# Kernel tuning notes

Hardware: AMD Instinct MI355X
Metric: run time of the kernel (lower is better)

The kernel has to match this reference:

```python
import jax, jax.numpy as jnp
import numpy as np

B, S = 16, 4096
E_ENC, E_DEC, H = 1024, 1024, 512


def setup_inputs() -> dict:
    key = jax.random.key(0)
    ks = jax.random.split(key, 8)
    sc_e = 1.0 / np.sqrt(E_ENC)
    sc_d = 1.0 / np.sqrt(E_DEC)
    sc_h = 1.0 / np.sqrt(H)
    return {
        "encoder_hiddens": jax.random.normal(ks[0], (B, S, E_ENC), jnp.float32),
        "decoder_hidden": jax.random.normal(ks[1], (B, E_DEC), jnp.float32),
        "We": jax.random.uniform(ks[2], (E_ENC, H), jnp.float32, -sc_e, sc_e),
        "be": jax.random.uniform(ks[3], (H,), jnp.float32, -sc_e, sc_e),
        "Wd": jax.random.uniform(ks[4], (E_DEC, H), jnp.float32, -sc_d, sc_d),
        "bd": jax.random.uniform(ks[5], (H,), jnp.float32, -sc_d, sc_d),
        "Wo": jax.random.uniform(ks[6], (H, 1), jnp.float32, -sc_h, sc_h),
        "bo": jax.random.uniform(ks[7], (1,), jnp.float32, -sc_h, sc_h),
    }


def reference(encoder_hiddens, decoder_hidden, We, be, Wd, bd, Wo, bo):
    # Additive (Bahdanau) attention.
    # enc_proj: [B,S,H]; dec_proj: [B,1,H] broadcast over sequence.
    enc_proj = jnp.einsum("bse,eh->bsh", encoder_hiddens, We) + be
    dec_proj = jnp.einsum("bd,dh->bh", decoder_hidden, Wd) + bd
    e = jnp.tanh(enc_proj + dec_proj[:, None, :])          # [B,S,H]
    scores = jnp.einsum("bsh,h->bs", e, Wo[:, 0]) + bo[0]  # [B,S]
    attn = jax.nn.softmax(scores, axis=-1)                 # [B,S]
    context = jnp.einsum("bs,bse->be", attn, encoder_hiddens)  # [B,E_ENC]
    return context
```

## Files before the change

### kernel.cpp

```cpp
#include <hip/hip_runtime.h>
#include <hip/hip_bf16.h>
#include <math.h>

#define B_ 16
#define S_ 4096
#define E_ 1024
#define H_ 512

typedef short bf16x8 __attribute__((ext_vector_type(8)));
typedef unsigned short u16x8 __attribute__((ext_vector_type(8)));
typedef float f32x4 __attribute__((ext_vector_type(4)));

__device__ inline unsigned short f2bf(float x) {
    __hip_bfloat16 h = __float2bfloat16(x);
    return *(unsigned short*)&h;
}

__global__ __launch_bounds__(256) void we_transpose_kernel(
    const float* __restrict__ We, unsigned short* __restrict__ WeT) {
    __shared__ float sT[64][65];
    int k0 = (blockIdx.x >> 3) * 64;
    int n0 = (blockIdx.x & 7) * 64;
    int t = threadIdx.x;
#pragma unroll
    for (int p = 0; p < 16; ++p) {
        int idx = p * 256 + t;
        int k = idx >> 6, n = idx & 63;
        sT[n][k] = We[(size_t)(k0 + k) * H_ + n0 + n];
    }
    __syncthreads();
#pragma unroll
    for (int p = 0; p < 16; ++p) {
        int idx = p * 256 + t;
        int n = idx >> 6, k = idx & 63;
        WeT[(size_t)(n0 + n) * E_ + k0 + k] = f2bf(sT[n][k]);
    }
}

__global__ __launch_bounds__(256) void dp_kernel(const float* __restrict__ dec,
                                                 const float* __restrict__ Wd,
                                                 const float* __restrict__ bd,
                                                 const float* __restrict__ be,
                                                 float* __restrict__ dp) {
    int b = blockIdx.x >> 3;
    int hc = blockIdx.x & 7;
    int t = threadIdx.x;
    int h = hc * 64 + (t & 63);
    int ec = t >> 6;
    const float* dr = dec + b * E_ + ec * 256;
    const float* wp = Wd + (size_t)(ec * 256) * H_ + h;
    float acc = 0.f;
#pragma unroll 8
    for (int e = 0; e < 256; ++e) acc = fmaf(dr[e], wp[(size_t)e * H_], acc);
    __shared__ float red[4][64];
    red[ec][t & 63] = acc;
    __syncthreads();
    if (t < 64) {
        int hh = hc * 64 + t;
        dp[b * H_ + hh] = red[0][t] + red[1][t] + red[2][t] + red[3][t] + bd[hh] + be[hh];
    }
}

#define BM 128
#define BN 128
#define BK 32
#define LDA 40

__global__ __launch_bounds__(256) void scores_mfma_kernel(
    const float* __restrict__ enc, const unsigned short* __restrict__ WeT,
    const float* __restrict__ Wo, const float* __restrict__ dp,
    float* __restrict__ parts) {
    __shared__ unsigned short sA[BM * LDA];
    __shared__ unsigned short sB[BN * LDA];
    __shared__ float sRed[2][BM];

    int tid = threadIdx.x;
    int nt = blockIdx.x & 3;
    int mt = blockIdx.x >> 2;
    int m0 = mt * BM;
    int n0 = nt * BN;
    int b = m0 >> 12;
    int wave = tid >> 6, lane = tid & 63;
    int wm = wave & 1, wn = wave >> 1;
    int quad = lane >> 4, l16 = lane & 15;

    f32x4 acc[4][4];
#pragma unroll
    for (int i = 0; i < 4; ++i)
#pragma unroll
        for (int j = 0; j < 4; ++j) acc[i][j] = (f32x4)0.f;

    int am = tid >> 3;
    int ac = (tid & 7) * 4;
    const float* encP = enc + (size_t)(m0 + am) * E_ + ac;
    unsigned short* sAp = sA + am * LDA + ac;
    int bn = tid >> 1, bh = tid & 1;
    const unsigned short* wtP = WeT + (size_t)(n0 + bn) * E_ + bh * 16;
    unsigned short* sBp = sB + bn * LDA + bh * 16;

    int aBase = (wm * 64 + l16) * LDA + quad * 8;
    int bBase = (wn * 64 + l16) * LDA + quad * 8;

    for (int k0 = 0; k0 < E_; k0 += BK) {
        __syncthreads();
#pragma unroll
        for (int p = 0; p < 4; ++p) {
            float4 v = *(const float4*)(encP + (size_t)p * 32 * E_ + k0);
            ushort4 u;
            u.x = f2bf(v.x); u.y = f2bf(v.y); u.z = f2bf(v.z); u.w = f2bf(v.w);
            *(ushort4*)(sAp + p * 32 * LDA) = u;
        }
        u16x8 w0 = *(const u16x8*)(wtP + k0);
        u16x8 w1 = *(const u16x8*)(wtP + k0 + 8);
        *(u16x8*)(sBp) = w0;
        *(u16x8*)(sBp + 8) = w1;
        __syncthreads();

        bf16x8 aR[4], bR[4];
#pragma unroll
        for (int i = 0; i < 4; ++i) aR[i] = *(const bf16x8*)(sA + aBase + i * 16 * LDA);
#pragma unroll
        for (int j = 0; j < 4; ++j) bR[j] = *(const bf16x8*)(sB + bBase + j * 16 * LDA);
#pragma unroll
        for (int i = 0; i < 4; ++i)
#pragma unroll
            for (int j = 0; j < 4; ++j)
                acc[i][j] = __builtin_amdgcn_mfma_f32_16x16x32_bf16(aR[i], bR[j], acc[i][j], 0, 0, 0);
    }

    float dpv[4], wov[4];
#pragma unroll
    for (int j = 0; j < 4; ++j) {
        int h = n0 + wn * 64 + j * 16 + l16;
        dpv[j] = dp[b * H_ + h];
        wov[j] = Wo[h];
    }
    float part[4][4];
#pragma unroll
    for (int i = 0; i < 4; ++i)
#pragma unroll
        for (int r = 0; r < 4; ++r) {
            float s = 0.f;
#pragma unroll
            for (int j = 0; j < 4; ++j) {
                float x = acc[i][j][r] + dpv[j];
                float e = __expf(2.f * x);
                s += (1.f - 2.f / (e + 1.f)) * wov[j];
            }
            part[i][r] = s;
        }
#pragma unroll
    for (int i = 0; i < 4; ++i)
#pragma unroll
        for (int r = 0; r < 4; ++r) {
            float s = part[i][r];
            s += __shfl_xor(s, 1, 64);
            s += __shfl_xor(s, 2, 64);
            s += __shfl_xor(s, 4, 64);
            s += __shfl_xor(s, 8, 64);
            part[i][r] = s;
        }
    if (l16 == 0) {
#pragma unroll
        for (int i = 0; i < 4; ++i)
#pragma unroll
            for (int r = 0; r < 4; ++r)
                sRed[wn][wm * 64 + i * 16 + quad * 4 + r] = part[i][r];
    }
    __syncthreads();
    if (tid < BM) {
        float sc = sRed[0][tid] + sRed[1][tid];
        int s = (m0 & (S_ - 1)) + tid;
        parts[(size_t)(nt * B_ + b) * S_ + s] = sc;
    }
}

__global__ __launch_bounds__(256) void softmax_kernel(float* __restrict__ parts) {
    int b = blockIdx.x;
    const float* p0 = parts + (size_t)(0 * B_ + b) * S_;
    const float* p1 = parts + (size_t)(1 * B_ + b) * S_;
    const float* p2 = parts + (size_t)(2 * B_ + b) * S_;
    const float* p3 = parts + (size_t)(3 * B_ + b) * S_;
    float* row = parts + (size_t)b * S_;
    int tid = threadIdx.x;
    float v[16];
    float m = -1e30f;
#pragma unroll
    for (int i = 0; i < 16; ++i) {
        int idx = i * 256 + tid;
        v[i] = p0[idx] + p1[idx] + p2[idx] + p3[idx];
        m = fmaxf(m, v[i]);
    }
    for (int off = 32; off; off >>= 1) m = fmaxf(m, __shfl_xor(m, off, 64));
    __shared__ float redm[4];
    __shared__ float reds[4];
    if ((tid & 63) == 0) redm[tid >> 6] = m;
    __syncthreads();
    m = fmaxf(fmaxf(redm[0], redm[1]), fmaxf(redm[2], redm[3]));
    float s = 0.f;
#pragma unroll
    for (int i = 0; i < 16; ++i) {
        v[i] = __expf(v[i] - m);
        s += v[i];
    }
    for (int off = 32; off; off >>= 1) s += __shfl_xor(s, off, 64);
    if ((tid & 63) == 0) reds[tid >> 6] = s;
    __syncthreads();
    s = reds[0] + reds[1] + reds[2] + reds[3];
    float inv = 1.f / s;
#pragma unroll
    for (int i = 0; i < 16; ++i) row[i * 256 + tid] = v[i] * inv;
}

__global__ __launch_bounds__(256) void zero_kernel(float* __restrict__ out) {
    out[blockIdx.x * 256 + threadIdx.x] = 0.f;
}

__global__ __launch_bounds__(256) void ctx_kernel(const float* __restrict__ enc,
                                                  const float* __restrict__ attn,
                                                  float* __restrict__ out) {
    int b = blockIdx.x >> 5;
    int s0 = (blockIdx.x & 31) * 128;
    int tid = threadIdx.x;
    __shared__ float w[128];
    if (tid < 128) w[tid] = attn[(size_t)b * S_ + s0 + tid];
    __syncthreads();
    const float* base = enc + ((size_t)b * S_ + s0) * E_ + tid * 4;
    float4 acc = make_float4(0.f, 0.f, 0.f, 0.f);
    for (int s = 0; s < 128; ++s) {
        float4 v = *(const float4*)(base + (size_t)s * E_);
        float ws = w[s];
        acc.x = fmaf(ws, v.x, acc.x);
        acc.y = fmaf(ws, v.y, acc.y);
        acc.z = fmaf(ws, v.z, acc.z);
        acc.w = fmaf(ws, v.w, acc.w);
    }
    float* o = out + b * E_ + tid * 4;
    atomicAdd(o + 0, acc.x);
    atomicAdd(o + 1, acc.y);
    atomicAdd(o + 2, acc.z);
    atomicAdd(o + 3, acc.w);
}

extern "C" void kernel_launch(void* const* d_in, const int* in_sizes, int n_in,
                              void* d_out, int out_size, void* d_ws, size_t ws_size,
                              hipStream_t stream) {
    const float* enc = (const float*)d_in[0];
    const float* dec = (const float*)d_in[1];
    const float* We  = (const float*)d_in[2];
    const float* be  = (const float*)d_in[3];
    const float* Wd  = (const float*)d_in[4];
    const float* bd  = (const float*)d_in[5];
    const float* Wo  = (const float*)d_in[6];
    float* out = (float*)d_out;

    char* w = (char*)d_ws;
    unsigned short* WeT = (unsigned short*)w;
    float* dp = (float*)(w + (1 << 20));
    float* parts = (float*)(w + (1 << 20) + 32768);
    float* attn = parts;

    we_transpose_kernel<<<128, 256, 0, stream>>>(We, WeT);
    dp_kernel<<<B_ * 8, 256, 0, stream>>>(dec, Wd, bd, be, dp);
    scores_mfma_kernel<<<(B_ * S_ / BM) * (H_ / BN), 256, 0, stream>>>(enc, WeT, Wo, dp, parts);
    softmax_kernel<<<B_, 256, 0, stream>>>(parts);
    zero_kernel<<<(B_ * E_) / 256, 256, 0, stream>>>(out);
    ctx_kernel<<<B_ * 32, 256, 0, stream>>>(enc, attn, out);
}
```

Measured before the change: 539.6 us.

## Give each scores block the full H width, stash a bf16 copy of enc, and reduce context in two passes

```diff
diff --git a/kernel.cpp b/kernel.cpp
--- a/kernel.cpp
+++ b/kernel.cpp
@@ -14,6 +14,12 @@
 __device__ inline unsigned short f2bf(float x) {
     __hip_bfloat16 h = __float2bfloat16(x);
     return *(unsigned short*)&h;
+}
+__device__ inline float bf2f(unsigned short u) {
+    unsigned int x = ((unsigned int)u) << 16;
+    float f;
+    __builtin_memcpy(&f, &x, 4);
+    return f;
 }
 
 __global__ __launch_bounds__(256) void we_transpose_kernel(
@@ -61,134 +67,112 @@
     }
 }
 
-#define BM 128
-#define BN 128
+#define BM 64
 #define BK 32
 #define LDA 40
 
-__global__ __launch_bounds__(256) void scores_mfma_kernel(
+template <int WRITE_ENCB>
+__global__ __launch_bounds__(256, 2) void scores_mfma_kernel(
     const float* __restrict__ enc, const unsigned short* __restrict__ WeT,
     const float* __restrict__ Wo, const float* __restrict__ dp,
-    float* __restrict__ parts) {
+    float* __restrict__ scores, unsigned short* __restrict__ encB) {
     __shared__ unsigned short sA[BM * LDA];
-    __shared__ unsigned short sB[BN * LDA];
-    __shared__ float sRed[2][BM];
+    __shared__ float sRed[4][BM];
 
     int tid = threadIdx.x;
-    int nt = blockIdx.x & 3;
-    int mt = blockIdx.x >> 2;
-    int m0 = mt * BM;
-    int n0 = nt * BN;
-    int b = m0 >> 12;
     int wave = tid >> 6, lane = tid & 63;
-    int wm = wave & 1, wn = wave >> 1;
     int quad = lane >> 4, l16 = lane & 15;
-
-    f32x4 acc[4][4];
+    size_t m0 = (size_t)blockIdx.x * BM;
+    int b = (int)(m0 >> 12);
+
+    int srow = tid >> 3;
+    int skoff = (tid & 7) * 4;
+    const float* encP = enc + (m0 + srow) * E_ + skoff;
+    unsigned short* encBP = encB + (m0 + srow) * E_ + skoff;
+    unsigned short* sAw = sA + srow * LDA + skoff;
+
+    f32x4 acc[4][8];
 #pragma unroll
     for (int i = 0; i < 4; ++i)
 #pragma unroll
-        for (int j = 0; j < 4; ++j) acc[i][j] = (f32x4)0.f;
-
-    int am = tid >> 3;
-    int ac = (tid & 7) * 4;
-    const float* encP = enc + (size_t)(m0 + am) * E_ + ac;
-    unsigned short* sAp = sA + am * LDA + ac;
-    int bn = tid >> 1, bh = tid & 1;
-    const unsigned short* wtP = WeT + (size_t)(n0 + bn) * E_ + bh * 16;
-    unsigned short* sBp = sB + bn * LDA + bh * 16;
-
-    int aBase = (wm * 64 + l16) * LDA + quad * 8;
-    int bBase = (wn * 64 + l16) * LDA + quad * 8;
+        for (int j = 0; j < 8; ++j) acc[i][j] = (f32x4)0.f;
+
+    float4 cur0 = *(const float4*)(encP);
+    float4 cur1 = *(const float4*)(encP + 32 * E_);
+
+    const unsigned short* wrow = WeT + (size_t)(wave * 128 + l16) * E_ + quad * 8;
 
     for (int k0 = 0; k0 < E_; k0 += BK) {
+        ushort4 u0, u1;
+        u0.x = f2bf(cur0.x); u0.y = f2bf(cur0.y); u0.z = f2bf(cur0.z); u0.w = f2bf(cur0.w);
+        u1.x = f2bf(cur1.x); u1.y = f2bf(cur1.y); u1.z = f2bf(cur1.z); u1.w = f2bf(cur1.w);
+        *(ushort4*)(sAw) = u0;
+        *(ushort4*)(sAw + 32 * LDA) = u1;
+        if (WRITE_ENCB) {
+            *(ushort4*)(encBP + k0) = u0;
+            *(ushort4*)(encBP + k0 + 32 * E_) = u1;
+        }
         __syncthreads();
-#pragma unroll
-        for (int p = 0; p < 4; ++p) {
-            float4 v = *(const float4*)(encP + (size_t)p * 32 * E_ + k0);
-            ushort4 u;
-            u.x = f2bf(v.x); u.y = f2bf(v.y); u.z = f2bf(v.z); u.w = f2bf(v.w);
-            *(ushort4*)(sAp + p * 32 * LDA) = u;
-        }
-        u16x8 w0 = *(const u16x8*)(wtP + k0);
-        u16x8 w1 = *(const u16x8*)(wtP + k0 + 8);
-        *(u16x8*)(sBp) = w0;
-        *(u16x8*)(sBp + 8) = w1;
+        if (k0 + BK < E_) {
+            cur0 = *(const float4*)(encP + k0 + BK);
+            cur1 = *(const float4*)(encP + k0 + BK + 32 * E_);
+        }
+        bf16x8 aR[4];
+#pragma unroll
+        for (int i = 0; i < 4; ++i)
+            aR[i] = *(const bf16x8*)(sA + (i * 16 + l16) * LDA + quad * 8);
+#pragma unroll
+        for (int j = 0; j < 8; ++j) {
+            bf16x8 bR = *(const bf16x8*)(wrow + (size_t)j * 16 * E_ + k0);
+#pragma unroll
+            for (int i = 0; i < 4; ++i)
+                acc[i][j] = __builtin_amdgcn_mfma_f32_16x16x32_bf16(aR[i], bR, acc[i][j], 0, 0, 0);
+        }
         __syncthreads();
-
-        bf16x8 aR[4], bR[4];
-#pragma unroll
-        for (int i = 0; i < 4; ++i) aR[i] = *(const bf16x8*)(sA + aBase + i * 16 * LDA);
-#pragma unroll
-        for (int j = 0; j < 4; ++j) bR[j] = *(const bf16x8*)(sB + bBase + j * 16 * LDA);
-#pragma unroll
-        for (int i = 0; i < 4; ++i)
-#pragma unroll
-            for (int j = 0; j < 4; ++j)
-                acc[i][j] = __builtin_amdgcn_mfma_f32_16x16x32_bf16(aR[i], bR[j], acc[i][j], 0, 0, 0);
-    }
-
-    float dpv[4], wov[4];
-#pragma unroll
-    for (int j = 0; j < 4; ++j) {
-        int h = n0 + wn * 64 + j * 16 + l16;
-        dpv[j] = dp[b * H_ + h];
+    }
+
+    float dpv[8], wov[8];
+    const float* dpb = dp + b * H_;
+#pragma unroll
+    for (int j = 0; j < 8; ++j) {
+        int h = wave * 128 + j * 16 + l16;
+        dpv[j] = dpb[h];
         wov[j] = Wo[h];
     }
-    float part[4][4];
 #pragma unroll
     for (int i = 0; i < 4; ++i)
 #pragma unroll
         for (int r = 0; r < 4; ++r) {
             float s = 0.f;
 #pragma unroll
-            for (int j = 0; j < 4; ++j) {
+            for (int j = 0; j < 8; ++j) {
                 float x = acc[i][j][r] + dpv[j];
                 float e = __expf(2.f * x);
                 s += (1.f - 2.f / (e + 1.f)) * wov[j];
             }
-            part[i][r] = s;
-        }
-#pragma unroll
-    for (int i = 0; i < 4; ++i)
-#pragma unroll
-        for (int r = 0; r < 4; ++r) {
-            float s = part[i][r];
             s += __shfl_xor(s, 1, 64);
             s += __shfl_xor(s, 2, 64);
             s += __shfl_xor(s, 4, 64);
             s += __shfl_xor(s, 8, 64);
-            part[i][r] = s;
-        }
-    if (l16 == 0) {
-#pragma unroll
-        for (int i = 0; i < 4; ++i)
-#pragma unroll
-            for (int r = 0; r < 4; ++r)
-                sRed[wn][wm * 64 + i * 16 + quad * 4 + r] = part[i][r];
-    }
+            if (l16 == 0) sRed[wave][i * 16 + quad * 4 + r] = s;
+        }
     __syncthreads();
     if (tid < BM) {
-        float sc = sRed[0][tid] + sRed[1][tid];
-        int s = (m0 & (S_ - 1)) + tid;
-        parts[(size_t)(nt * B_ + b) * S_ + s] = sc;
-    }
-}
-
-__global__ __launch_bounds__(256) void softmax_kernel(float* __restrict__ parts) {
+        int s_in = (int)(m0 & (S_ - 1)) + tid;
+        scores[(size_t)b * S_ + s_in] =
+            sRed[0][tid] + sRed[1][tid] + sRed[2][tid] + sRed[3][tid];
+    }
+}
+
+__global__ __launch_bounds__(256) void softmax_kernel(float* __restrict__ sc) {
     int b = blockIdx.x;
-    const float* p0 = parts + (size_t)(0 * B_ + b) * S_;
-    const float* p1 = parts + (size_t)(1 * B_ + b) * S_;
-    const float* p2 = parts + (size_t)(2 * B_ + b) * S_;
-    const float* p3 = parts + (size_t)(3 * B_ + b) * S_;
-    float* row = parts + (size_t)b * S_;
+    float* row = sc + (size_t)b * S_;
     int tid = threadIdx.x;
     float v[16];
     float m = -1e30f;
 #pragma unroll
     for (int i = 0; i < 16; ++i) {
-        int idx = i * 256 + tid;
-        v[i] = p0[idx] + p1[idx] + p2[idx] + p3[idx];
+        v[i] = row[i * 256 + tid];
         m = fmaxf(m, v[i]);
     }
     for (int off = 32; off; off >>= 1) m = fmaxf(m, __shfl_xor(m, off, 64));
@@ -212,34 +196,75 @@
     for (int i = 0; i < 16; ++i) row[i * 256 + tid] = v[i] * inv;
 }
 
-__global__ __launch_bounds__(256) void zero_kernel(float* __restrict__ out) {
-    out[blockIdx.x * 256 + threadIdx.x] = 0.f;
-}
-
-__global__ __launch_bounds__(256) void ctx_kernel(const float* __restrict__ enc,
-                                                  const float* __restrict__ attn,
-                                                  float* __restrict__ out) {
+__global__ __launch_bounds__(256) void ctx_partial_bf16(
+    const unsigned short* __restrict__ encB, const float* __restrict__ attn,
+    float* __restrict__ part) {
     int b = blockIdx.x >> 5;
-    int s0 = (blockIdx.x & 31) * 128;
+    int c = blockIdx.x & 31;
+    int s0 = c * 128;
     int tid = threadIdx.x;
     __shared__ float w[128];
     if (tid < 128) w[tid] = attn[(size_t)b * S_ + s0 + tid];
     __syncthreads();
+    int e8 = (tid & 127) * 8;
+    int sh = tid >> 7;
+    const unsigned short* base = encB + ((size_t)b * S_ + s0 + sh * 64) * E_ + e8;
+    const float* wp = w + sh * 64;
+    float acc[8];
+#pragma unroll
+    for (int t = 0; t < 8; ++t) acc[t] = 0.f;
+    for (int s = 0; s < 64; s += 4) {
+        u16x8 v0 = *(const u16x8*)(base + (size_t)(s + 0) * E_);
+        u16x8 v1 = *(const u16x8*)(base + (size_t)(s + 1) * E_);
+        u16x8 v2 = *(const u16x8*)(base + (size_t)(s + 2) * E_);
+        u16x8 v3 = *(const u16x8*)(base + (size_t)(s + 3) * E_);
+        float w0 = wp[s], w1 = wp[s + 1], w2 = wp[s + 2], w3 = wp[s + 3];
+#pragma unroll
+        for (int t = 0; t < 8; ++t) {
+            acc[t] = fmaf(w0, bf2f(v0[t]), acc[t]);
+            acc[t] = fmaf(w1, bf2f(v1[t]), acc[t]);
+            acc[t] = fmaf(w2, bf2f(v2[t]), acc[t]);
+            acc[t] = fmaf(w3, bf2f(v3[t]), acc[t]);
+        }
+    }
+    float* po = part + ((size_t)(b * 64 + c * 2 + sh)) * E_ + e8;
+    *(float4*)(po) = make_float4(acc[0], acc[1], acc[2], acc[3]);
+    *(float4*)(po + 4) = make_float4(acc[4], acc[5], acc[6], acc[7]);
+}
+
+__global__ __launch_bounds__(256) void ctx_partial_f32(
+    const float* __restrict__ enc, const float* __restrict__ attn,
+    float* __restrict__ part) {
+    int b = blockIdx.x >> 5;
+    int c = blockIdx.x & 31;
+    int s0 = c * 128;
+    int tid = threadIdx.x;
+    __shared__ float w[128];
+    if (tid < 128) w[tid] = attn[(size_t)b * S_ + s0 + tid];
+    __syncthreads();
     const float* base = enc + ((size_t)b * S_ + s0) * E_ + tid * 4;
     float4 acc = make_float4(0.f, 0.f, 0.f, 0.f);
-    for (int s = 0; s < 128; ++s) {
-        float4 v = *(const float4*)(base + (size_t)s * E_);
-        float ws = w[s];
-        acc.x = fmaf(ws, v.x, acc.x);
-        acc.y = fmaf(ws, v.y, acc.y);
-        acc.z = fmaf(ws, v.z, acc.z);
-        acc.w = fmaf(ws, v.w, acc.w);
-    }
-    float* o = out + b * E_ + tid * 4;
-    atomicAdd(o + 0, acc.x);
-    atomicAdd(o + 1, acc.y);
-    atomicAdd(o + 2, acc.z);
-    atomicAdd(o + 3, acc.w);
+    for (int s = 0; s < 128; s += 2) {
+        float4 v0 = *(const float4*)(base + (size_t)s * E_);
+        float4 v1 = *(const float4*)(base + (size_t)(s + 1) * E_);
+        float w0 = w[s], w1 = w[s + 1];
+        acc.x = fmaf(w0, v0.x, acc.x); acc.y = fmaf(w0, v0.y, acc.y);
+        acc.z = fmaf(w0, v0.z, acc.z); acc.w = fmaf(w0, v0.w, acc.w);
+        acc.x = fmaf(w1, v1.x, acc.x); acc.y = fmaf(w1, v1.y, acc.y);
+        acc.z = fmaf(w1, v1.z, acc.z); acc.w = fmaf(w1, v1.w, acc.w);
+    }
+    *(float4*)(part + ((size_t)(b * 32 + c)) * E_ + tid * 4) = acc;
+}
+
+__global__ __launch_bounds__(256) void ctx_reduce(const float* __restrict__ part,
+                                                  float* __restrict__ out, int nch) {
+    int idx = blockIdx.x * 256 + threadIdx.x;
+    int b = idx >> 10;
+    int e = idx & 1023;
+    const float* p = part + (size_t)b * nch * E_ + e;
+    float s = 0.f;
+    for (int c = 0; c < nch; ++c) s += p[(size_t)c * E_];
+    out[idx] = s;
 }
 
 extern "C" void kernel_launch(void* const* d_in, const int* in_sizes, int n_in,
@@ -257,13 +282,23 @@
     char* w = (char*)d_ws;
     unsigned short* WeT = (unsigned short*)w;
     float* dp = (float*)(w + (1 << 20));
-    float* parts = (float*)(w + (1 << 20) + 32768);
-    float* attn = parts;
+    float* scores = (float*)(w + (1 << 20) + (32 << 10));
+    float* part = (float*)(w + (2 << 20));
+    unsigned short* encB = (unsigned short*)(w + (8 << 20));
+    const size_t need_bf16 = (size_t)(8 << 20) + (size_t)B_ * S_ * E_ * 2;
+    bool use_bf16_ctx = ws_size >= need_bf16;
 
     we_transpose_kernel<<<128, 256, 0, stream>>>(We, WeT);
     dp_kernel<<<B_ * 8, 256, 0, stream>>>(dec, Wd, bd, be, dp);
-    scores_mfma_kernel<<<(B_ * S_ / BM) * (H_ / BN), 256, 0, stream>>>(enc, WeT, Wo, dp, parts);
-    softmax_kernel<<<B_, 256, 0, stream>>>(parts);
-    zero_kernel<<<(B_ * E_) / 256, 256, 0, stream>>>(out);
-    ctx_kernel<<<B_ * 32, 256, 0, stream>>>(enc, attn, out);
-}
+    if (use_bf16_ctx) {
+        scores_mfma_kernel<1><<<B_ * S_ / BM, 256, 0, stream>>>(enc, WeT, Wo, dp, scores, encB);
+        softmax_kernel<<<B_, 256, 0, stream>>>(scores);
+        ctx_partial_bf16<<<B_ * 32, 256, 0, stream>>>(encB, scores, part);
+        ctx_reduce<<<B_ * E_ / 256, 256, 0, stream>>>(part, out, 64);
+    } else {
+        scores_mfma_kernel<0><<<B_ * S_ / BM, 256, 0, stream>>>(enc, WeT, Wo, dp, scores, encB);
+        softmax_kernel<<<B_, 256, 0, stream>>>(scores);
+        ctx_partial_f32<<<B_ * 32, 256, 0, stream>>>(enc, scores, part);
+        ctx_reduce<<<B_ * E_ / 256, 256, 0, stream>>>(part, out, 32);
+    }
+}
```

Result: slower. 572.1 us (+6.0%).
